# Optimization experiments

Measured on AMD Instinct MI355X. Metric: run time of the kernel, lower is better.

Reference implementation:

```python
import jax, jax.numpy as jnp
import numpy as np

M, K, N = 8192, 4096, 4096  # tokens, in_features, out_features


def setup_inputs() -> dict:
    key = jax.random.key(0)
    k1, k2, k3, k4 = jax.random.split(key, 4)
    inp = jax.random.normal(k1, (M, K), dtype=jnp.float32)
    # int8-range weights stored as int32 host-side; [out_features, in_features] like torch Linear
    weight = jax.random.randint(k2, (N, K), -128, 128, dtype=jnp.int32)
    weight_scale = jax.random.uniform(k3, (N,), dtype=jnp.float32, minval=1e-3, maxval=2e-2)
    bias = jax.random.normal(k4, (N,), dtype=jnp.float32)
    return {"input": inp, "weight": weight, "weight_scale": weight_scale, "bias": bias}


def reference(input, weight, weight_scale, bias):
    # --- init-time transforms (W8A8IntLinear.__init__) ---
    wq = weight.T.astype(jnp.int8)                                   # [K, N]
    azp_adj = jnp.sum(wq.astype(jnp.int32), axis=0, keepdims=True)    # [1, N] int32 column sums

    # --- dynamic asymmetric per-token int8 quantization (scaled_int8_quant) ---
    x_max = jnp.max(input, axis=-1, keepdims=True)                    # [M, 1]
    x_min = jnp.min(input, axis=-1, keepdims=True)                    # [M, 1]
    scale = (x_max - x_min) / 255.0                                   # per-token scale
    azp = jnp.round(-128.0 - x_min / scale).astype(jnp.int32)         # per-token zero point
    q = jnp.clip(jnp.round(input / scale).astype(jnp.int32) + azp, -128, 127).astype(jnp.int8)

    # --- int8 GEMM with int32 accumulation (cutlass_scaled_mm_azp) ---
    acc = jnp.matmul(q, wq, preferred_element_type=jnp.int32)         # [M, N] int32
    corrected = (acc - azp * azp_adj).astype(jnp.float32)             # zero-point correction
    return scale * weight_scale[None, :] * corrected + bias[None, :]
```

## Files before the change

### kernel.cpp

```cpp
#include <hip/hip_runtime.h>
#include <cstdint>
#include <cstddef>


#define M_DIM 8192
#define K_DIM 4096
#define N_DIM 4096
#define NT 64

typedef int v4i __attribute__((ext_vector_type(4)));

__global__ __launch_bounds__(256) void prep_kernel(
    const float* __restrict__ x, signed char* __restrict__ q,
    float* __restrict__ scale_out, int* __restrict__ azp_out,
    const int* __restrict__ w, signed char* __restrict__ w8,
    int* __restrict__ azp_adj)
{
    const int t = threadIdx.x;
    if (blockIdx.x < M_DIM) {
        const int m = blockIdx.x;
        const float4* row4 = (const float4*)(x + (size_t)m * K_DIM);

        float4 v[4];
        float mx = -3.4e38f, mn = 3.4e38f;
#pragma unroll
        for (int i = 0; i < 4; ++i) {
            v[i] = row4[i * 256 + t];
            mx = fmaxf(mx, fmaxf(fmaxf(v[i].x, v[i].y), fmaxf(v[i].z, v[i].w)));
            mn = fminf(mn, fminf(fminf(v[i].x, v[i].y), fminf(v[i].z, v[i].w)));
        }
#pragma unroll
        for (int off = 32; off; off >>= 1) {
            mx = fmaxf(mx, __shfl_down(mx, off));
            mn = fminf(mn, __shfl_down(mn, off));
        }
        __shared__ float smx[4], smn[4];
        if ((t & 63) == 0) { smx[t >> 6] = mx; smn[t >> 6] = mn; }
        __syncthreads();
        mx = fmaxf(fmaxf(smx[0], smx[1]), fmaxf(smx[2], smx[3]));
        mn = fminf(fminf(smn[0], smn[1]), fminf(smn[2], smn[3]));

        const float scale = (mx - mn) / 255.0f;
        const int azp = (int)rintf(-128.0f - mn / scale);
        if (t == 0) { scale_out[m] = scale; azp_out[m] = azp; }

        int* qrow = (int*)(q + (size_t)m * K_DIM);
        const float* vf = (const float*)v;
#pragma unroll
        for (int i = 0; i < 4; ++i) {
            int b[4];
#pragma unroll
            for (int j = 0; j < 4; ++j) {
                int qv = (int)rintf(vf[4 * i + j] / scale) + azp;
                qv = qv < -128 ? -128 : (qv > 127 ? 127 : qv);
                b[j] = qv;
            }
            qrow[i * 256 + t] =
                (b[0] & 255) | ((b[1] & 255) << 8) | ((b[2] & 255) << 16) | ((b[3] & 255) << 24);
        }
    } else {
        const int n = blockIdx.x - M_DIM;
        const int4* row = (const int4*)(w + (size_t)n * K_DIM);
        int* w8row = (int*)(w8 + (size_t)n * K_DIM);
        int sum = 0;
#pragma unroll
        for (int i = 0; i < 4; ++i) {
            int4 a = row[i * 256 + t];
            sum += a.x + a.y + a.z + a.w;
            w8row[i * 256 + t] =
                (a.x & 255) | ((a.y & 255) << 8) | ((a.z & 255) << 16) | ((a.w & 255) << 24);
        }
#pragma unroll
        for (int off = 32; off; off >>= 1) sum += __shfl_down(sum, off);
        __shared__ int ssum[4];
        if ((t & 63) == 0) ssum[t >> 6] = sum;
        __syncthreads();
        if (t == 0) azp_adj[n] = ssum[0] + ssum[1] + ssum[2] + ssum[3];
    }
}

__device__ __forceinline__ void async_copy16(const signed char* g, signed char* l) {
    __builtin_amdgcn_global_load_lds(
        (const __attribute__((address_space(1))) void*)g,
        (__attribute__((address_space(3))) void*)l, 16, 0, 0);
}

template<int RO>
__device__ __forceinline__ void mfma16(const v4i (&x)[4], const v4i (&y)[4], v4i (&acc)[8][4]) {
#pragma unroll
    for (int i = 0; i < 4; ++i)
#pragma unroll
        for (int j = 0; j < 4; ++j)
            acc[RO + i][j] = __builtin_amdgcn_mfma_i32_16x16x64_i8(x[i], y[j], acc[RO + i][j], 0, 0, 0);
}

template<int CUR, bool STG, int VMN, bool RA>
__device__ __forceinline__ void tile_body(
    int kt, signed char (*sA)[16384], signed char (*sB)[16384],
    const signed char* ag0, const signed char* ag1,
    const signed char* bg0, const signed char* bg1,
    int t, int aIdx, int bIdx,
    v4i (&af)[4], v4i (&bf)[4],
    v4i (&afn)[4], v4i (&bfn)[4],
    v4i (&acc)[8][4])
{
    const v4i* a4 = (const v4i*)&sA[CUR][0];

    if constexpr (STG) {
        const int ko = (kt + 3) << 6;
        signed char* dA = &sA[(CUR + 3) & 3][0];
        signed char* dB = &sB[(CUR + 3) & 3][0];
        async_copy16(ag0 + ko, dA + t * 16);
        async_copy16(ag1 + ko, dA + 8192 + t * 16);
        async_copy16(bg0 + ko, dB + t * 16);
        async_copy16(bg1 + ko, dB + 8192 + t * 16);
    }
    v4i ah[4];
#pragma unroll
    for (int i = 0; i < 4; ++i) ah[i] = a4[aIdx + 256 + i * 64];
    if constexpr (VMN == 8)      asm volatile("s_waitcnt vmcnt(8)" ::: "memory");
    else if constexpr (VMN == 4) asm volatile("s_waitcnt vmcnt(4)" ::: "memory");
    else if constexpr (VMN == 0) asm volatile("s_waitcnt vmcnt(0)" ::: "memory");
    asm volatile("s_barrier" ::: "memory");
    asm volatile("s_waitcnt lgkmcnt(4)" ::: "memory");
    __builtin_amdgcn_sched_barrier(0);
    __builtin_amdgcn_s_setprio(1);
    mfma16<0>(af, bf, acc);
    __builtin_amdgcn_s_setprio(0);
    asm volatile("s_barrier" ::: "memory");

    if constexpr (RA) {
        const v4i* a4n = (const v4i*)&sA[(CUR + 1) & 3][0];
        const v4i* b4n = (const v4i*)&sB[(CUR + 1) & 3][0];
#pragma unroll
        for (int i = 0; i < 4; ++i) {
            afn[i] = a4n[aIdx + i * 64];
            bfn[i] = b4n[bIdx + i * 64];
        }
        asm volatile("s_waitcnt lgkmcnt(8)" ::: "memory");
    } else {
        asm volatile("s_waitcnt lgkmcnt(0)" ::: "memory");
    }
    __builtin_amdgcn_sched_barrier(0);
    __builtin_amdgcn_s_setprio(1);
    mfma16<4>(ah, bf, acc);
    __builtin_amdgcn_s_setprio(0);
    asm volatile("s_barrier" ::: "memory");
}

__global__ __launch_bounds__(512, 2) void gemm_kernel(
    const signed char* __restrict__ A,
    const signed char* __restrict__ B,
    const float* __restrict__ scale, const int* __restrict__ azp,
    const int* __restrict__ azp_adj, const float* __restrict__ wscale,
    const float* __restrict__ bias, float* __restrict__ out)
{
    __shared__ signed char sA[4][16384];
    __shared__ signed char sB[4][16384];

    const int t = threadIdx.x;
    const int lane = t & 63;
    const int wave = t >> 6;
    const int quad = lane >> 4;
    const int r16 = lane & 15;

    int bid = blockIdx.y * gridDim.x + blockIdx.x;
    bid = (bid & 7) * 64 + (bid >> 3);
    const int bn = (bid & 15) << 8;
    const int bm = (bid >> 4) << 8;

    const int wm = (wave >> 2) << 7;
    const int wn = (wave & 3) << 6;

    v4i acc[8][4];
#pragma unroll
    for (int i = 0; i < 8; ++i)
#pragma unroll
        for (int j = 0; j < 4; ++j) acc[i][j] = (v4i){0, 0, 0, 0};

    const int srow = t >> 2;
    const int scol = ((t & 3) ^ ((t >> 3) & 3)) << 4;
    const signed char* ag0 = A + (size_t)(bm + srow) * K_DIM + scol;
    const signed char* ag1 = A + (size_t)(bm + 128 + srow) * K_DIM + scol;
    const signed char* bg0 = B + (size_t)(bn + srow) * K_DIM + scol;
    const signed char* bg1 = B + (size_t)(bn + 128 + srow) * K_DIM + scol;

#define STAGE_A(kt) do { const int _b = (kt) & 3; const int _ko = (kt) << 6; \
    async_copy16(ag0 + _ko, &sA[_b][t * 16]); \
    async_copy16(ag1 + _ko, &sA[_b][8192 + t * 16]); } while (0)
#define STAGE_B(kt) do { const int _b = (kt) & 3; const int _ko = (kt) << 6; \
    async_copy16(bg0 + _ko, &sB[_b][t * 16]); \
    async_copy16(bg1 + _ko, &sB[_b][8192 + t * 16]); } while (0)

    const int swz = quad ^ ((r16 >> 1) & 3);
    const int aIdx = (wm + r16) * 4 + swz;
    const int bIdx = (wn + r16) * 4 + swz;

    STAGE_A(0); STAGE_B(0);
    STAGE_A(1); STAGE_B(1);
    STAGE_A(2); STAGE_B(2);
    asm volatile("s_waitcnt vmcnt(8)" ::: "memory");
    asm volatile("s_barrier" ::: "memory");

    v4i afA[4], bfA[4], afB[4], bfB[4];
    {
        const v4i* a4 = (const v4i*)&sA[0][0];
        const v4i* b4 = (const v4i*)&sB[0][0];
#pragma unroll
        for (int i = 0; i < 4; ++i) {
            afA[i] = a4[aIdx + i * 64];
            bfA[i] = b4[bIdx + i * 64];
        }
    }

    for (int kt = 0; kt < NT - 4; kt += 4) {
        tile_body<0, true, 8, true>(kt,     sA, sB, ag0, ag1, bg0, bg1, t, aIdx, bIdx, afA, bfA, afB, bfB, acc);
        tile_body<1, true, 8, true>(kt + 1, sA, sB, ag0, ag1, bg0, bg1, t, aIdx, bIdx, afB, bfB, afA, bfA, acc);
        tile_body<2, true, 8, true>(kt + 2, sA, sB, ag0, ag1, bg0, bg1, t, aIdx, bIdx, afA, bfA, afB, bfB, acc);
        tile_body<3, true, 8, true>(kt + 3, sA, sB, ag0, ag1, bg0, bg1, t, aIdx, bIdx, afB, bfB, afA, bfA, acc);
    }
    tile_body<0, true,  8, true >(NT - 4, sA, sB, ag0, ag1, bg0, bg1, t, aIdx, bIdx, afA, bfA, afB, bfB, acc);
    tile_body<1, false, 4, true >(NT - 3, sA, sB, ag0, ag1, bg0, bg1, t, aIdx, bIdx, afB, bfB, afA, bfA, acc);
    tile_body<2, false, 0, true >(NT - 2, sA, sB, ag0, ag1, bg0, bg1, t, aIdx, bIdx, afA, bfA, afB, bfB, acc);
    tile_body<3, false, -1, false>(NT - 1, sA, sB, ag0, ag1, bg0, bg1, t, aIdx, bIdx, afB, bfB, afA, bfA, acc);

#undef STAGE_A
#undef STAGE_B

#pragma unroll
    for (int i = 0; i < 8; ++i) {
        const int mbase = bm + wm + i * 16 + quad * 4;
        float sm[4]; int am[4];
#pragma unroll
        for (int r = 0; r < 4; ++r) { sm[r] = scale[mbase + r]; am[r] = azp[mbase + r]; }
#pragma unroll
        for (int j = 0; j < 4; ++j) {
            const int n = bn + wn + j * 16 + r16;
            const float wsn = wscale[n];
            const int adjn = azp_adj[n];
            const float bn_ = bias[n];
#pragma unroll
            for (int r = 0; r < 4; ++r) {
                const int c = acc[i][j][r] - am[r] * adjn;
                out[(size_t)(mbase + r) * N_DIM + n] = sm[r] * wsn * (float)c + bn_;
            }
        }
    }
}

extern "C" void kernel_launch(void* const* d_in, const int* in_sizes, int n_in,
                              void* d_out, int out_size, void* d_ws, size_t ws_size,
                              hipStream_t stream) {
    const float* x      = (const float*)d_in[0];
    const int*   w      = (const int*)d_in[1];
    const float* wscale = (const float*)d_in[2];
    const float* bias   = (const float*)d_in[3];
    float* out = (float*)d_out;

    char* ws = (char*)d_ws;
    signed char* q8  = (signed char*)ws;
    signed char* w8  = (signed char*)(ws + 33554432);
    float* scl       = (float*)(ws + 50331648);
    int*   azp       = (int*)(ws + 50331648 + 32768);
    int*   adj       = (int*)(ws + 50331648 + 65536);

    prep_kernel<<<M_DIM + N_DIM, 256, 0, stream>>>(x, q8, scl, azp, w, w8, adj);
    dim3 grid(N_DIM / 256, M_DIM / 256);
    gemm_kernel<<<grid, 512, 0, stream>>>(q8, w8, scl, azp, adj, wscale, bias, out);
}
```

Baseline: 402.4 us.

## Drop register double-buffering of LDS fragments and merge MFMA halves per tile

Each tile now loads its own A and B fragments from LDS at the start, instead of prefetching the next tile's fragments into a second register set mid-tile. Both MFMA groups run back-to-back after a single lgkmcnt(0) wait, cutting the barriers per tile from three to two. This frees registers and removes a synchronisation point. In exchange, LDS read latency is no longer hidden behind the previous tile's MFMAs, which may expose stalls at each tile start.

```diff
diff --git a/kernel.cpp b/kernel.cpp
--- a/kernel.cpp
+++ b/kernel.cpp
@@ -94,17 +94,25 @@
             acc[RO + i][j] = __builtin_amdgcn_mfma_i32_16x16x64_i8(x[i], y[j], acc[RO + i][j], 0, 0, 0);
 }
 
-template<int CUR, bool STG, int VMN, bool RA>
+template<int CUR, bool STG, int VMN>
 __device__ __forceinline__ void tile_body(
     int kt, signed char (*sA)[16384], signed char (*sB)[16384],
     const signed char* ag0, const signed char* ag1,
     const signed char* bg0, const signed char* bg1,
-    int t, int aIdx, int bIdx,
-    v4i (&af)[4], v4i (&bf)[4],
-    v4i (&afn)[4], v4i (&bfn)[4],
-    v4i (&acc)[8][4])
+    int t, int aIdx, int bIdx, v4i (&acc)[8][4])
 {
     const v4i* a4 = (const v4i*)&sA[CUR][0];
+    const v4i* b4 = (const v4i*)&sB[CUR][0];
+
+    v4i af[4], bf[4], ah[4];
+#pragma unroll
+    for (int i = 0; i < 4; ++i) {
+        af[i] = a4[aIdx + i * 64];
+        bf[i] = b4[bIdx + i * 64];
+    }
+#pragma unroll
+    for (int i = 0; i < 4; ++i)
+        ah[i] = a4[aIdx + 256 + i * 64];
 
     if constexpr (STG) {
         const int ko = (kt + 3) << 6;
@@ -115,37 +123,20 @@
         async_copy16(bg0 + ko, dB + t * 16);
         async_copy16(bg1 + ko, dB + 8192 + t * 16);
     }
-    v4i ah[4];
-#pragma unroll
-    for (int i = 0; i < 4; ++i) ah[i] = a4[aIdx + 256 + i * 64];
+
+    asm volatile("s_barrier" ::: "memory");
+    asm volatile("s_waitcnt lgkmcnt(0)" ::: "memory");
+    __builtin_amdgcn_sched_barrier(0);
+    __builtin_amdgcn_s_setprio(1);
+    mfma16<0>(af, bf, acc);
+    mfma16<4>(ah, bf, acc);
+    __builtin_amdgcn_s_setprio(0);
+
     if constexpr (VMN == 8)      asm volatile("s_waitcnt vmcnt(8)" ::: "memory");
     else if constexpr (VMN == 4) asm volatile("s_waitcnt vmcnt(4)" ::: "memory");
     else if constexpr (VMN == 0) asm volatile("s_waitcnt vmcnt(0)" ::: "memory");
-    asm volatile("s_barrier" ::: "memory");
-    asm volatile("s_waitcnt lgkmcnt(4)" ::: "memory");
-    __builtin_amdgcn_sched_barrier(0);
-    __builtin_amdgcn_s_setprio(1);
-    mfma16<0>(af, bf, acc);
-    __builtin_amdgcn_s_setprio(0);
-    asm volatile("s_barrier" ::: "memory");
-
-    if constexpr (RA) {
-        const v4i* a4n = (const v4i*)&sA[(CUR + 1) & 3][0];
-        const v4i* b4n = (const v4i*)&sB[(CUR + 1) & 3][0];
-#pragma unroll
-        for (int i = 0; i < 4; ++i) {
-            afn[i] = a4n[aIdx + i * 64];
-            bfn[i] = b4n[bIdx + i * 64];
-        }
-        asm volatile("s_waitcnt lgkmcnt(8)" ::: "memory");
-    } else {
-        asm volatile("s_waitcnt lgkmcnt(0)" ::: "memory");
-    }
-    __builtin_amdgcn_sched_barrier(0);
-    __builtin_amdgcn_s_setprio(1);
-    mfma16<4>(ah, bf, acc);
-    __builtin_amdgcn_s_setprio(0);
-    asm volatile("s_barrier" ::: "memory");
+    if constexpr (VMN >= 0)
+        asm volatile("s_barrier" ::: "memory");
 }
 
 __global__ __launch_bounds__(512, 2) void gemm_kernel(
@@ -202,27 +193,16 @@
     asm volatile("s_waitcnt vmcnt(8)" ::: "memory");
     asm volatile("s_barrier" ::: "memory");
 
-    v4i afA[4], bfA[4], afB[4], bfB[4];
-    {
-        const v4i* a4 = (const v4i*)&sA[0][0];
-        const v4i* b4 = (const v4i*)&sB[0][0];
-#pragma unroll
-        for (int i = 0; i < 4; ++i) {
-            afA[i] = a4[aIdx + i * 64];
-            bfA[i] = b4[bIdx + i * 64];
-        }
-    }
-
     for (int kt = 0; kt < NT - 4; kt += 4) {
-        tile_body<0, true, 8, true>(kt,     sA, sB, ag0, ag1, bg0, bg1, t, aIdx, bIdx, afA, bfA, afB, bfB, acc);
-        tile_body<1, true, 8, true>(kt + 1, sA, sB, ag0, ag1, bg0, bg1, t, aIdx, bIdx, afB, bfB, afA, bfA, acc);
-        tile_body<2, true, 8, true>(kt + 2, sA, sB, ag0, ag1, bg0, bg1, t, aIdx, bIdx, afA, bfA, afB, bfB, acc);
-        tile_body<3, true, 8, true>(kt + 3, sA, sB, ag0, ag1, bg0, bg1, t, aIdx, bIdx, afB, bfB, afA, bfA, acc);
-    }
-    tile_body<0, true,  8, true >(NT - 4, sA, sB, ag0, ag1, bg0, bg1, t, aIdx, bIdx, afA, bfA, afB, bfB, acc);
-    tile_body<1, false, 4, true >(NT - 3, sA, sB, ag0, ag1, bg0, bg1, t, aIdx, bIdx, afB, bfB, afA, bfA, acc);
-    tile_body<2, false, 0, true >(NT - 2, sA, sB, ag0, ag1, bg0, bg1, t, aIdx, bIdx, afA, bfA, afB, bfB, acc);
-    tile_body<3, false, -1, false>(NT - 1, sA, sB, ag0, ag1, bg0, bg1, t, aIdx, bIdx, afB, bfB, afA, bfA, acc);
+        tile_body<0, true, 8>(kt,     sA, sB, ag0, ag1, bg0, bg1, t, aIdx, bIdx, acc);
+        tile_body<1, true, 8>(kt + 1, sA, sB, ag0, ag1, bg0, bg1, t, aIdx, bIdx, acc);
+        tile_body<2, true, 8>(kt + 2, sA, sB, ag0, ag1, bg0, bg1, t, aIdx, bIdx, acc);
+        tile_body<3, true, 8>(kt + 3, sA, sB, ag0, ag1, bg0, bg1, t, aIdx, bIdx, acc);
+    }
+    tile_body<0, true,  8>(NT - 4, sA, sB, ag0, ag1, bg0, bg1, t, aIdx, bIdx, acc);
+    tile_body<1, false, 4>(NT - 3, sA, sB, ag0, ag1, bg0, bg1, t, aIdx, bIdx, acc);
+    tile_body<2, false, 0>(NT - 2, sA, sB, ag0, ag1, bg0, bg1, t, aIdx, bIdx, acc);
+    tile_body<3, false, -1>(NT - 1, sA, sB, ag0, ag1, bg0, bg1, t, aIdx, bIdx, acc);
 
 #undef STAGE_A
 #undef STAGE_B
```

Result: no change. 395.8 us (-1.6%).
